# Kernel tuning notes

Measured on AMD Instinct MI355X. Metric: run time of the kernel, lower is better.

## Reference

```python
import jax, jax.numpy as jnp
import numpy as np

B = 1_000_000
N_DIR, N_TRIAL = 2, 4
ALPHA, R_GAS, EPS = 0.3, 8.314462618, 1e-12
TAU_CLIP, LN_CLIP = 10.0, 20.0
EPS_FD, SIGMA, MARGIN = 1e-4, 0.05, 0.0
LAM_PHY, LAM_GD, LAM_TPD = 1.0, 0.1, 0.1


def renorm3(x):
    # clamp to >=0 and normalize so components sum to 1 (last axis)
    x = jnp.maximum(x, 0.0)
    return x / jnp.maximum(x.sum(-1, keepdims=True), EPS)


def nrtl_ln_gamma(x, T, g):
    # x: (B,3), T: (B,), g: (B,3,3) -> ln_gamma: (B,3)
    x = jnp.maximum(x, 0.0)
    Tc = jnp.maximum(T, 1.0)
    tau = jnp.clip(g / (R_GAS * jnp.maximum(Tc, EPS)[:, None, None]), -TAU_CLIP, TAU_CLIP)
    G = jnp.exp(-ALPHA * tau)
    denom = jnp.maximum(jnp.einsum('bj,bji->bi', x, G), EPS)          # (B,3)
    A = jnp.einsum('bj,bji->bi', x, tau * G)                          # (B,3), == num1 in torch
    term1 = A / denom
    W = x[:, None, :] * G / denom[:, None, :]                         # (B,3,3)
    inside = tau - (A / denom)[:, None, :]
    term2 = (W * inside).sum(-1)
    return jnp.clip(term1 + term2, -LN_CLIP, LN_CLIP)


def setup_inputs() -> dict:
    key = jax.random.key(0)
    k1, k2, k3, k4, k5, k6 = jax.random.split(key, 6)
    pred = jax.random.uniform(k1, (B, 6), dtype=jnp.float32, minval=0.01, maxval=1.0)
    target = jax.random.uniform(k2, (B, 6), dtype=jnp.float32, minval=0.01, maxval=1.0)
    T = 298.0 + 100.0 * jax.random.uniform(k3, (B,), dtype=jnp.float32)  # Kelvin
    g = 800.0 * jax.random.normal(k4, (B, 3, 3), dtype=jnp.float32)      # J/mol
    # simplex directions: zero-sum, unit-norm (matches _sample_simplex_directions)
    v = jax.random.normal(k5, (N_DIR, B, 3), dtype=jnp.float32)
    v = v - v.mean(-1, keepdims=True)
    dirs = v / jnp.maximum(jnp.linalg.norm(v, axis=-1, keepdims=True), 1e-12)
    noise = SIGMA * jax.random.normal(k6, (N_TRIAL, B, 3), dtype=jnp.float32)
    return {'pred': pred, 'target': target, 'T': T, 'g': g, 'dirs': dirs, 'noise': noise}


def reference(pred, target, T, g, dirs, noise):
    # supervised MSE on (E+R) compositions
    L_sup = jnp.mean((pred - target) ** 2)

    xE = renorm3(pred[:, :3])
    xR = renorm3(pred[:, 3:])
    ln_gE = nrtl_ln_gamma(xE, T, g)
    ln_gR = nrtl_ln_gamma(xR, T, g)
    # chemical potential residual r_k = ln(xE_k gE_k) - ln(xR_k gR_k)
    r = jnp.log(jnp.maximum(xE, EPS)) + ln_gE - (jnp.log(jnp.maximum(xR, EPS)) + ln_gR)
    L_phy = jnp.mean(r ** 2)

    lg = jax.vmap(lambda xx: nrtl_ln_gamma(xx, T, g))  # over trial/direction axis

    # Gibbs-Duhem finite-difference penalty along simplex directions
    x_p = renorm3(xE[None] + EPS_FD * dirs)            # (N_DIR,B,3)
    x_m = renorm3(xE[None] - EPS_FD * dirs)
    d_ln = (lg(x_p) - lg(x_m)) / (2.0 * EPS_FD)
    gd = (xE[None] * d_ln).sum(-1)                     # (N_DIR,B)
    L_gd = jnp.mean(gd * gd)

    # TPD stability penalty
    w = renorm3(xE[None] + noise)                      # (N_TRIAL,B,3)
    ln_gw = lg(w)
    tpd = (w * (jnp.log(jnp.maximum(w, EPS)) + ln_gw
                - jnp.log(jnp.maximum(xE, EPS))[None] - ln_gE[None])).sum(-1)
    L_tpd = jnp.mean(jnp.maximum(MARGIN - tpd, 0.0))

    return L_sup + LAM_PHY * L_phy + LAM_GD * L_gd + LAM_TPD * L_tpd
```

## Files before the change

kernel.cpp:

```cpp
#include <hip/hip_runtime.h>


constexpr float ALPHA    = 0.3f;
constexpr float R_GAS    = 8.314462618f;
constexpr float EPS      = 1e-12f;
constexpr float TAU_CLIP = 10.0f;
constexpr float LN_CLIP  = 20.0f;
constexpr float EPS_FD   = 1e-4f;

constexpr float LOG2E = 1.44269504088896340736f;
constexpr float LN2   = 0.69314718055994530942f;

typedef float v2f __attribute__((ext_vector_type(2)));
typedef float v4f __attribute__((ext_vector_type(4)));

__device__ __forceinline__ float clipf(float v, float lo, float hi) {
    return fminf(fmaxf(v, lo), hi);
}
__device__ __forceinline__ float fast_rcp(float x) { return __builtin_amdgcn_rcpf(x); }
__device__ __forceinline__ v2f nt_load2(const float* p) {
    return __builtin_nontemporal_load((const v2f*)p);
}
__device__ __forceinline__ v4f nt_load4(const float* p) {
    return __builtin_nontemporal_load((const v4f*)p);
}
__device__ __forceinline__ float nt_load(const float* p) {
    return __builtin_nontemporal_load(p);
}

struct Mats {
    float tau[3][3];
    float G[3][3];
    float tG[3][3];
};

struct SIn {
    float p[6];
    float t[6];
    float T;
    float g[9];
    float dv[2][3];
    float nv[4][3];
};

__device__ __forceinline__ void ln_gamma3(const float x[3], const Mats& M, float lg[3]) {
    float ratio[3], c[3];
#pragma unroll
    for (int i = 0; i < 3; ++i) {
        float d = x[0] * M.G[0][i] + x[1] * M.G[1][i] + x[2] * M.G[2][i];
        d = fmaxf(d, EPS);
        float A = x[0] * M.tG[0][i] + x[1] * M.tG[1][i] + x[2] * M.tG[2][i];
        float inv = fast_rcp(d);
        ratio[i] = A * inv;
        c[i] = x[i] * inv;
    }
#pragma unroll
    for (int i = 0; i < 3; ++i) {
        float s = ratio[i];
#pragma unroll
        for (int j = 0; j < 3; ++j) {
            s += c[j] * (M.tG[i][j] - M.G[i][j] * ratio[j]);
        }
        lg[i] = clipf(s, -LN_CLIP, LN_CLIP);
    }
}

__device__ __forceinline__ void renorm3(float x[3]) {
    x[0] = fmaxf(x[0], 0.0f);
    x[1] = fmaxf(x[1], 0.0f);
    x[2] = fmaxf(x[2], 0.0f);
    float inv = fast_rcp(fmaxf(x[0] + x[1] + x[2], EPS));
    x[0] *= inv; x[1] *= inv; x[2] *= inv;
}

__device__ __forceinline__ float sample_contrib(const SIn& in) {
    float sup;
    {
        float d0 = in.p[0] - in.t[0], d1 = in.p[1] - in.t[1];
        float d2 = in.p[2] - in.t[2], d3 = in.p[3] - in.t[3];
        float d4 = in.p[4] - in.t[4], d5 = in.p[5] - in.t[5];
        sup = d0 * d0 + d1 * d1 + d2 * d2 + d3 * d3 + d4 * d4 + d5 * d5;
    }

    float xE[3] = {in.p[0], in.p[1], in.p[2]};
    float xR[3] = {in.p[3], in.p[4], in.p[5]};
    renorm3(xE);
    renorm3(xR);

    const float Tc = fmaxf(in.T, 1.0f);
    const float invRT = fast_rcp(R_GAS * Tc);
    Mats M;
#pragma unroll
    for (int a = 0; a < 3; ++a) {
#pragma unroll
        for (int b = 0; b < 3; ++b) {
            float ta = clipf(in.g[a * 3 + b] * invRT, -TAU_CLIP, TAU_CLIP);
            float Gv = __builtin_amdgcn_exp2f((-ALPHA * LOG2E) * ta);
            M.tau[a][b] = ta;
            M.G[a][b]   = Gv;
            M.tG[a][b]  = ta * Gv;
        }
    }

    float lgE[3], lgR[3];
    ln_gamma3(xE, M, lgE);
    ln_gamma3(xR, M, lgR);

    float logxE[3];
    float phy = 0.0f;
#pragma unroll
    for (int k = 0; k < 3; ++k) {
        logxE[k] = LN2 * __builtin_amdgcn_logf(fmaxf(xE[k], EPS));
        float logxR = LN2 * __builtin_amdgcn_logf(fmaxf(xR[k], EPS));
        float r = logxE[k] + lgE[k] - logxR - lgR[k];
        phy += r * r;
    }

    float gdsum = 0.0f;
#pragma unroll
    for (int d = 0; d < 2; ++d) {
        float xp[3], xm[3];
#pragma unroll
        for (int k = 0; k < 3; ++k) {
            xp[k] = xE[k] + EPS_FD * in.dv[d][k];
            xm[k] = xE[k] - EPS_FD * in.dv[d][k];
        }
        renorm3(xp);
        renorm3(xm);
        float lgp[3], lgm[3];
        ln_gamma3(xp, M, lgp);
        ln_gamma3(xm, M, lgm);
        float gd = 0.0f;
#pragma unroll
        for (int k = 0; k < 3; ++k) gd += xE[k] * (lgp[k] - lgm[k]);
        gd *= 0.5f / EPS_FD;
        gdsum += gd * gd;
    }

    float base[3];
#pragma unroll
    for (int k = 0; k < 3; ++k) base[k] = logxE[k] + lgE[k];

    float tpdsum = 0.0f;
#pragma unroll
    for (int tr = 0; tr < 4; ++tr) {
        float w[3];
#pragma unroll
        for (int k = 0; k < 3; ++k) w[k] = xE[k] + in.nv[tr][k];
        renorm3(w);
        float lgw[3];
        ln_gamma3(w, M, lgw);
        float tpd = 0.0f;
#pragma unroll
        for (int k = 0; k < 3; ++k) {
            float logw = LN2 * __builtin_amdgcn_logf(fmaxf(w[k], EPS));
            tpd += w[k] * (logw + lgw[k] - base[k]);
        }
        tpdsum += fmaxf(-tpd, 0.0f);
    }

    return sup * (1.0f / 6.0f)
         + phy * (1.0f / 3.0f)
         + 0.05f * gdsum
         + 0.025f * tpdsum;
}

__global__ __launch_bounds__(256, 3) void nrtl_loss_kernel(
    const float* __restrict__ pred,
    const float* __restrict__ target,
    const float* __restrict__ Tarr,
    const float* __restrict__ g,
    const float* __restrict__ dirs,
    const float* __restrict__ noise,
    float* __restrict__ partials, int B)
{
    const int t  = blockIdx.x * blockDim.x + threadIdx.x;
    const int i0 = t * 2;
    float contrib = 0.0f;

    if (i0 + 1 < B) {
        SIn in[2];

        {
            const float* prow = pred + (size_t)i0 * 6;
            v4f P0 = nt_load4(prow);
            v4f P1 = nt_load4(prow + 4);
            v4f P2 = nt_load4(prow + 8);
            in[0].p[0]=P0.x; in[0].p[1]=P0.y; in[0].p[2]=P0.z; in[0].p[3]=P0.w;
            in[0].p[4]=P1.x; in[0].p[5]=P1.y;
            in[1].p[0]=P1.z; in[1].p[1]=P1.w;
            in[1].p[2]=P2.x; in[1].p[3]=P2.y; in[1].p[4]=P2.z; in[1].p[5]=P2.w;
        }
        {
            const float* trow = target + (size_t)i0 * 6;
            v4f T0 = nt_load4(trow);
            v4f T1 = nt_load4(trow + 4);
            v4f T2 = nt_load4(trow + 8);
            in[0].t[0]=T0.x; in[0].t[1]=T0.y; in[0].t[2]=T0.z; in[0].t[3]=T0.w;
            in[0].t[4]=T1.x; in[0].t[5]=T1.y;
            in[1].t[0]=T1.z; in[1].t[1]=T1.w;
            in[1].t[2]=T2.x; in[1].t[3]=T2.y; in[1].t[4]=T2.z; in[1].t[5]=T2.w;
        }
        {
            v2f Tv = nt_load2(Tarr + i0);
            in[0].T = Tv.x; in[1].T = Tv.y;
        }
        {
            const float* grow = g + (size_t)i0 * 9;
            float gg[18];
#pragma unroll
            for (int j = 0; j < 9; ++j) {
                v2f gv = nt_load2(grow + 2 * j);
                gg[2 * j]     = gv.x;
                gg[2 * j + 1] = gv.y;
            }
#pragma unroll
            for (int k = 0; k < 9; ++k) { in[0].g[k] = gg[k]; in[1].g[k] = gg[9 + k]; }
        }
#pragma unroll
        for (int d = 0; d < 2; ++d) {
            const float* drow = dirs + ((size_t)d * B + i0) * 3;
            v2f a = nt_load2(drow);
            v2f b = nt_load2(drow + 2);
            v2f c = nt_load2(drow + 4);
            in[0].dv[d][0]=a.x; in[0].dv[d][1]=a.y; in[0].dv[d][2]=b.x;
            in[1].dv[d][0]=b.y; in[1].dv[d][1]=c.x; in[1].dv[d][2]=c.y;
        }
#pragma unroll
        for (int tr = 0; tr < 4; ++tr) {
            const float* nrow = noise + ((size_t)tr * B + i0) * 3;
            v2f a = nt_load2(nrow);
            v2f b = nt_load2(nrow + 2);
            v2f c = nt_load2(nrow + 4);
            in[0].nv[tr][0]=a.x; in[0].nv[tr][1]=a.y; in[0].nv[tr][2]=b.x;
            in[1].nv[tr][0]=b.y; in[1].nv[tr][1]=c.x; in[1].nv[tr][2]=c.y;
        }

        contrib = sample_contrib(in[0]) + sample_contrib(in[1]);
        contrib *= 1.0f / (float)B;
    } else if (i0 < B) {
        SIn in;
        const float* prow = pred   + (size_t)i0 * 6;
        const float* trow = target + (size_t)i0 * 6;
        const float* grow = g      + (size_t)i0 * 9;
#pragma unroll
        for (int k = 0; k < 6; ++k) { in.p[k] = nt_load(prow + k); in.t[k] = nt_load(trow + k); }
        in.T = nt_load(Tarr + i0);
#pragma unroll
        for (int k = 0; k < 9; ++k) in.g[k] = nt_load(grow + k);
#pragma unroll
        for (int d = 0; d < 2; ++d) {
            const float* drow = dirs + ((size_t)d * B + i0) * 3;
#pragma unroll
            for (int k = 0; k < 3; ++k) in.dv[d][k] = nt_load(drow + k);
        }
#pragma unroll
        for (int tr = 0; tr < 4; ++tr) {
            const float* nrow = noise + ((size_t)tr * B + i0) * 3;
#pragma unroll
            for (int k = 0; k < 3; ++k) in.nv[tr][k] = nt_load(nrow + k);
        }
        contrib = sample_contrib(in) * (1.0f / (float)B);
    }

#pragma unroll
    for (int off = 32; off > 0; off >>= 1)
        contrib += __shfl_down(contrib, off, 64);

    __shared__ float ssum[4];
    const int lane = threadIdx.x & 63;
    const int wid  = threadIdx.x >> 6;
    if (lane == 0) ssum[wid] = contrib;
    __syncthreads();
    if (threadIdx.x == 0) {
        partials[blockIdx.x] = ssum[0] + ssum[1] + ssum[2] + ssum[3];
    }
}

__global__ __launch_bounds__(256) void reduce_kernel(
    const float* __restrict__ partials, int n, float* __restrict__ out)
{
    double sacc = 0.0;
    for (int j = threadIdx.x; j < n; j += 256) sacc += (double)partials[j];
#pragma unroll
    for (int off = 32; off > 0; off >>= 1)
        sacc += __shfl_down(sacc, off, 64);
    __shared__ double ds[4];
    const int lane = threadIdx.x & 63;
    const int wid  = threadIdx.x >> 6;
    if (lane == 0) ds[wid] = sacc;
    __syncthreads();
    if (threadIdx.x == 0) out[0] = (float)(ds[0] + ds[1] + ds[2] + ds[3]);
}

extern "C" void kernel_launch(void* const* d_in, const int* in_sizes, int n_in,
                              void* d_out, int out_size, void* d_ws, size_t ws_size,
                              hipStream_t stream) {
    const float* pred   = (const float*)d_in[0];
    const float* target = (const float*)d_in[1];
    const float* Tarr   = (const float*)d_in[2];
    const float* g      = (const float*)d_in[3];
    const float* dirs   = (const float*)d_in[4];
    const float* noise  = (const float*)d_in[5];
    const int B = in_sizes[2];

    float* partials = (float*)d_ws;
    float* out      = (float*)d_out;

    const int block   = 256;
    const int pairs   = (B + 1) / 2;
    const int grid    = (pairs + block - 1) / block;
    nrtl_loss_kernel<<<grid, block, 0, stream>>>(pred, target, Tarr, g, dirs, noise, partials, B);
    reduce_kernel<<<1, block, 0, stream>>>(partials, grid, out);
}
```

Baseline: 185.1 us.

## Stage per-block inputs through LDS with coalesced 16-byte loads, one sample per thread

Each block of 256 samples now cooperatively loads all of its input arrays with fully coalesced 16-byte nontemporal loads into a 40KB shared buffer. After a barrier, each thread reads its own sample's fields from LDS. This replaces the earlier scheme where each thread loaded two samples with strided 8/16-byte loads. The grid doubles because each thread now handles one sample instead of two, and the min-waves launch bound is dropped. The LDS footprint and the barrier may limit occupancy and add latency, and there is less per-thread ILP.

```diff
diff --git a/kernel.cpp b/kernel.cpp
--- a/kernel.cpp
+++ b/kernel.cpp
@@ -11,16 +11,12 @@
 constexpr float LOG2E = 1.44269504088896340736f;
 constexpr float LN2   = 0.69314718055994530942f;
 
-typedef float v2f __attribute__((ext_vector_type(2)));
 typedef float v4f __attribute__((ext_vector_type(4)));
 
 __device__ __forceinline__ float clipf(float v, float lo, float hi) {
     return fminf(fmaxf(v, lo), hi);
 }
 __device__ __forceinline__ float fast_rcp(float x) { return __builtin_amdgcn_rcpf(x); }
-__device__ __forceinline__ v2f nt_load2(const float* p) {
-    return __builtin_nontemporal_load((const v2f*)p);
-}
 __device__ __forceinline__ v4f nt_load4(const float* p) {
     return __builtin_nontemporal_load((const v4f*)p);
 }
@@ -165,7 +161,7 @@
          + 0.025f * tpdsum;
 }
 
-__global__ __launch_bounds__(256, 3) void nrtl_loss_kernel(
+__global__ __launch_bounds__(256) void nrtl_loss_kernel(
     const float* __restrict__ pred,
     const float* __restrict__ target,
     const float* __restrict__ Tarr,
@@ -174,93 +170,120 @@
     const float* __restrict__ noise,
     float* __restrict__ partials, int B)
 {
-    const int t  = blockIdx.x * blockDim.x + threadIdx.x;
-    const int i0 = t * 2;
+    constexpr int OFF_T  = 6144;
+    constexpr int OFF_TP = 12288;
+    constexpr int OFF_G  = 13312;
+    constexpr int OFF_D  = 22528;
+    constexpr int OFF_N  = 28672;
+
+    __shared__ __align__(16) char smem[40960];
+    const int tid = threadIdx.x;
+    const int s0  = blockIdx.x << 8;
+
     float contrib = 0.0f;
 
-    if (i0 + 1 < B) {
-        SIn in[2];
-
+    if (s0 + 256 <= B) {
+        const float* gp = pred   + (size_t)s0 * 6;
+        const float* gt = target + (size_t)s0 * 6;
+        const float* gT = Tarr   + s0;
+        const float* gG = g      + (size_t)s0 * 9;
+
+        v4f vp0 = nt_load4(gp + tid * 4);
+        v4f vt0 = nt_load4(gt + tid * 4);
+        v4f vg0 = nt_load4(gG + tid * 4);
+        v4f vg1 = nt_load4(gG + (256 + tid) * 4);
+        v4f vp1, vt1, vT4, vg2;
+        if (tid < 128) {
+            vp1 = nt_load4(gp + (256 + tid) * 4);
+            vt1 = nt_load4(gt + (256 + tid) * 4);
+        }
+        if (tid < 64) {
+            vT4 = nt_load4(gT + tid * 4);
+            vg2 = nt_load4(gG + (512 + tid) * 4);
+        }
+        v4f vd0, vd1, vn0, vn1, vn2, vn3;
+        if (tid < 192) {
+            vd0 = nt_load4(dirs  + ((size_t)0 * B + s0) * 3 + tid * 4);
+            vd1 = nt_load4(dirs  + ((size_t)1 * B + s0) * 3 + tid * 4);
+            vn0 = nt_load4(noise + ((size_t)0 * B + s0) * 3 + tid * 4);
+            vn1 = nt_load4(noise + ((size_t)1 * B + s0) * 3 + tid * 4);
+            vn2 = nt_load4(noise + ((size_t)2 * B + s0) * 3 + tid * 4);
+            vn3 = nt_load4(noise + ((size_t)3 * B + s0) * 3 + tid * 4);
+        }
+
+        char* sw = smem + tid * 16;
+        *(v4f*)(sw)                = vp0;
+        *(v4f*)(sw + OFF_T)        = vt0;
+        *(v4f*)(sw + OFF_G)        = vg0;
+        *(v4f*)(sw + OFF_G + 4096) = vg1;
+        if (tid < 128) {
+            *(v4f*)(sw + 4096)         = vp1;
+            *(v4f*)(sw + OFF_T + 4096) = vt1;
+        }
+        if (tid < 64) {
+            *(v4f*)(sw + OFF_TP)       = vT4;
+            *(v4f*)(sw + OFF_G + 8192) = vg2;
+        }
+        if (tid < 192) {
+            *(v4f*)(sw + OFF_D)        = vd0;
+            *(v4f*)(sw + OFF_D + 3072) = vd1;
+            *(v4f*)(sw + OFF_N)        = vn0;
+            *(v4f*)(sw + OFF_N + 3072) = vn1;
+            *(v4f*)(sw + OFF_N + 6144) = vn2;
+            *(v4f*)(sw + OFF_N + 9216) = vn3;
+        }
+        __syncthreads();
+
+        SIn in;
         {
-            const float* prow = pred + (size_t)i0 * 6;
-            v4f P0 = nt_load4(prow);
-            v4f P1 = nt_load4(prow + 4);
-            v4f P2 = nt_load4(prow + 8);
-            in[0].p[0]=P0.x; in[0].p[1]=P0.y; in[0].p[2]=P0.z; in[0].p[3]=P0.w;
-            in[0].p[4]=P1.x; in[0].p[5]=P1.y;
-            in[1].p[0]=P1.z; in[1].p[1]=P1.w;
-            in[1].p[2]=P2.x; in[1].p[3]=P2.y; in[1].p[4]=P2.z; in[1].p[5]=P2.w;
-        }
-        {
-            const float* trow = target + (size_t)i0 * 6;
-            v4f T0 = nt_load4(trow);
-            v4f T1 = nt_load4(trow + 4);
-            v4f T2 = nt_load4(trow + 8);
-            in[0].t[0]=T0.x; in[0].t[1]=T0.y; in[0].t[2]=T0.z; in[0].t[3]=T0.w;
-            in[0].t[4]=T1.x; in[0].t[5]=T1.y;
-            in[1].t[0]=T1.z; in[1].t[1]=T1.w;
-            in[1].t[2]=T2.x; in[1].t[3]=T2.y; in[1].t[4]=T2.z; in[1].t[5]=T2.w;
-        }
-        {
-            v2f Tv = nt_load2(Tarr + i0);
-            in[0].T = Tv.x; in[1].T = Tv.y;
-        }
-        {
-            const float* grow = g + (size_t)i0 * 9;
-            float gg[18];
-#pragma unroll
-            for (int j = 0; j < 9; ++j) {
-                v2f gv = nt_load2(grow + 2 * j);
-                gg[2 * j]     = gv.x;
-                gg[2 * j + 1] = gv.y;
+            const float* LP = (const float*)(smem)          + tid * 6;
+            const float* LT = (const float*)(smem + OFF_T)  + tid * 6;
+#pragma unroll
+            for (int k = 0; k < 6; ++k) { in.p[k] = LP[k]; in.t[k] = LT[k]; }
+            in.T = ((const float*)(smem + OFF_TP))[tid];
+            const float* LG = (const float*)(smem + OFF_G)  + tid * 9;
+#pragma unroll
+            for (int k = 0; k < 9; ++k) in.g[k] = LG[k];
+#pragma unroll
+            for (int d = 0; d < 2; ++d) {
+                const float* LD = (const float*)(smem + OFF_D + 3072 * d) + tid * 3;
+#pragma unroll
+                for (int k = 0; k < 3; ++k) in.dv[d][k] = LD[k];
             }
 #pragma unroll
-            for (int k = 0; k < 9; ++k) { in[0].g[k] = gg[k]; in[1].g[k] = gg[9 + k]; }
-        }
-#pragma unroll
-        for (int d = 0; d < 2; ++d) {
-            const float* drow = dirs + ((size_t)d * B + i0) * 3;
-            v2f a = nt_load2(drow);
-            v2f b = nt_load2(drow + 2);
-            v2f c = nt_load2(drow + 4);
-            in[0].dv[d][0]=a.x; in[0].dv[d][1]=a.y; in[0].dv[d][2]=b.x;
-            in[1].dv[d][0]=b.y; in[1].dv[d][1]=c.x; in[1].dv[d][2]=c.y;
-        }
-#pragma unroll
-        for (int tr = 0; tr < 4; ++tr) {
-            const float* nrow = noise + ((size_t)tr * B + i0) * 3;
-            v2f a = nt_load2(nrow);
-            v2f b = nt_load2(nrow + 2);
-            v2f c = nt_load2(nrow + 4);
-            in[0].nv[tr][0]=a.x; in[0].nv[tr][1]=a.y; in[0].nv[tr][2]=b.x;
-            in[1].nv[tr][0]=b.y; in[1].nv[tr][1]=c.x; in[1].nv[tr][2]=c.y;
-        }
-
-        contrib = sample_contrib(in[0]) + sample_contrib(in[1]);
-        contrib *= 1.0f / (float)B;
-    } else if (i0 < B) {
-        SIn in;
-        const float* prow = pred   + (size_t)i0 * 6;
-        const float* trow = target + (size_t)i0 * 6;
-        const float* grow = g      + (size_t)i0 * 9;
-#pragma unroll
-        for (int k = 0; k < 6; ++k) { in.p[k] = nt_load(prow + k); in.t[k] = nt_load(trow + k); }
-        in.T = nt_load(Tarr + i0);
-#pragma unroll
-        for (int k = 0; k < 9; ++k) in.g[k] = nt_load(grow + k);
-#pragma unroll
-        for (int d = 0; d < 2; ++d) {
-            const float* drow = dirs + ((size_t)d * B + i0) * 3;
-#pragma unroll
-            for (int k = 0; k < 3; ++k) in.dv[d][k] = nt_load(drow + k);
-        }
-#pragma unroll
-        for (int tr = 0; tr < 4; ++tr) {
-            const float* nrow = noise + ((size_t)tr * B + i0) * 3;
-#pragma unroll
-            for (int k = 0; k < 3; ++k) in.nv[tr][k] = nt_load(nrow + k);
+            for (int tr = 0; tr < 4; ++tr) {
+                const float* LN = (const float*)(smem + OFF_N + 3072 * tr) + tid * 3;
+#pragma unroll
+                for (int k = 0; k < 3; ++k) in.nv[tr][k] = LN[k];
+            }
         }
         contrib = sample_contrib(in) * (1.0f / (float)B);
+    } else {
+        const int i = s0 + tid;
+        if (i < B) {
+            SIn in;
+            const float* prow = pred   + (size_t)i * 6;
+            const float* trow = target + (size_t)i * 6;
+            const float* grow = g      + (size_t)i * 9;
+#pragma unroll
+            for (int k = 0; k < 6; ++k) { in.p[k] = nt_load(prow + k); in.t[k] = nt_load(trow + k); }
+            in.T = nt_load(Tarr + i);
+#pragma unroll
+            for (int k = 0; k < 9; ++k) in.g[k] = nt_load(grow + k);
+#pragma unroll
+            for (int d = 0; d < 2; ++d) {
+                const float* drow = dirs + ((size_t)d * B + i) * 3;
+#pragma unroll
+                for (int k = 0; k < 3; ++k) in.dv[d][k] = nt_load(drow + k);
+            }
+#pragma unroll
+            for (int tr = 0; tr < 4; ++tr) {
+                const float* nrow = noise + ((size_t)tr * B + i) * 3;
+#pragma unroll
+                for (int k = 0; k < 3; ++k) in.nv[tr][k] = nt_load(nrow + k);
+            }
+            contrib = sample_contrib(in) * (1.0f / (float)B);
+        }
     }
 
 #pragma unroll
@@ -307,9 +330,8 @@
     float* partials = (float*)d_ws;
     float* out      = (float*)d_out;
 
-    const int block   = 256;
-    const int pairs   = (B + 1) / 2;
-    const int grid    = (pairs + block - 1) / block;
+    const int block = 256;
+    const int grid  = (B + block - 1) / block;
     nrtl_loss_kernel<<<grid, block, 0, stream>>>(pred, target, Tarr, g, dirs, noise, partials, B);
     reduce_kernel<<<1, block, 0, stream>>>(partials, grid, out);
 }
```

After: 167.7 us. 1.1x faster.
